# Performance work log

Measured on AMD Instinct MI355X. Metric: run time of the kernel, lower is better.

## Reference

```python
import jax, jax.numpy as jnp
import numpy as np

B, N, C, H, W = 32, 32, 3, 32, 32
HID, OUT = 256, 128


def _conv(x, w, b):
    y = jax.lax.conv_general_dilated(
        x, w, window_strides=(1, 1), padding="SAME",
        dimension_numbers=("NCHW", "OIHW", "NCHW"))
    return y + b[None, :, None, None]


def _sage(h, lw, lb, rw):
    # PyG SAGEConv with mean aggregation on a fully-connected graph (no self-loops):
    # agg_i = (sum_j h_j - h_i) / (N-1); out = agg @ lw.T + lb + h @ rw.T
    n = h.shape[1]
    agg = (jnp.sum(h, axis=1, keepdims=True) - h) / (n - 1)
    return jnp.einsum('bnd,od->bno', agg, lw) + lb + jnp.einsum('bnd,od->bno', h, rw)


def setup_inputs() -> dict:
    key = jax.random.key(0)
    ks = jax.random.split(key, 16)
    def g(k, shape, scale):
        return jax.random.normal(k, shape, dtype=jnp.float32) * scale
    return {
        "x": jax.random.normal(ks[0], (B, N, C, H, W), dtype=jnp.float32),
        "mask": jnp.ones((B, N), dtype=jnp.float32),
        "conv1_w": g(ks[1], (64, C, 3, 3), 0.1),
        "conv1_b": jnp.zeros((64,), jnp.float32),
        "conv2_w": g(ks[2], (128, 64, 3, 3), 0.05),
        "conv2_b": jnp.zeros((128,), jnp.float32),
        "fc_w": g(ks[3], (HID, 128), 0.08),
        "fc_b": jnp.zeros((HID,), jnp.float32),
        "s1_lw": g(ks[4], (HID, HID), 0.06),
        "s1_lb": jnp.zeros((HID,), jnp.float32),
        "s1_rw": g(ks[5], (HID, HID), 0.06),
        "s2_lw": g(ks[6], (OUT, HID), 0.06),
        "s2_lb": jnp.zeros((OUT,), jnp.float32),
        "s2_rw": g(ks[7], (OUT, HID), 0.06),
    }


def reference(x, mask, conv1_w, conv1_b, conv2_w, conv2_b, fc_w, fc_b,
              s1_lw, s1_lb, s1_rw, s2_lw, s2_lb, s2_rw):
    b, n, c, h, w = x.shape
    z = x.reshape(b * n, c, h, w)
    z = jax.nn.relu(_conv(z, conv1_w, conv1_b))
    z = jax.nn.relu(_conv(z, conv2_w, conv2_b))
    z = jnp.mean(z, axis=(2, 3))                      # AdaptiveAvgPool2d((1,1)) + flatten
    z = z @ fc_w.T + fc_b                             # [B*N, HID]
    z = z.reshape(b, n, -1) * mask[:, :, None]
    z = jax.nn.relu(_sage(z, s1_lw, s1_lb, s1_rw))
    z = _sage(z, s2_lw, s2_lb, s2_rw)                 # [B, N, OUT]
    return z
```

## Files before the change

kernel.cpp:

```cpp
#include <hip/hip_runtime.h>
#include <hip/hip_bf16.h>


typedef __attribute__((ext_vector_type(8))) short bfrag;
typedef __attribute__((ext_vector_type(4))) float f32x4;
typedef __attribute__((ext_vector_type(16))) float f32x16;

static __device__ __forceinline__ unsigned short f2bf(float f) {
    union { float f; unsigned u; } v; v.f = f;
    unsigned r = v.u + 0x7fff + ((v.u >> 16) & 1);
    return (unsigned short)(r >> 16);
}

static __device__ __forceinline__ unsigned cvtpk(float lo, float hi) {
    unsigned r;
    asm("v_cvt_pk_bf16_f32 %0, %1, %2" : "=v"(r) : "v"(lo), "v"(hi));
    return r;
}

static __device__ __forceinline__ void gl_lds16(const short* g, short* l) {
    __builtin_amdgcn_global_load_lds(
        (const __attribute__((address_space(1))) unsigned int*)g,
        (__attribute__((address_space(3))) unsigned int*)l, 16, 0, 0);
}

__global__ __launch_bounds__(256) void prep_kernel(
    const float* __restrict__ s1lw, const float* __restrict__ s1rw,
    const float* __restrict__ s2lw, const float* __restrict__ s2rw,
    const float* __restrict__ c2w, const float* __restrict__ c1w,
    const float* __restrict__ c1b, const float* __restrict__ fcw,
    float* __restrict__ l1T, float* __restrict__ w1pT,
    float* __restrict__ l2T, float* __restrict__ w2pT,
    float* __restrict__ fwT,
    short* __restrict__ w2c, short* __restrict__ w1b) {
    int i = blockIdx.x * 256 + threadIdx.x;
    const float inv31 = 1.f / 31.f;
    if (i < 65536) {
        int d = i >> 8, o = i & 255;
        float lw = s1lw[o * 256 + d];
        l1T[i]  = lw;
        w1pT[i] = s1rw[o * 256 + d] - lw * inv31;
    }
    if (i < 32768) {
        int d = i >> 7, o = i & 127;
        float lw = s2lw[o * 256 + d];
        l2T[i]  = lw;
        w2pT[i] = s2rw[o * 256 + d] - lw * inv31;
        int c = i >> 8, o2 = i & 255;
        fwT[i] = fcw[o2 * 128 + c];
    }
    if (i < 73728) {
        int tap = i >> 13, r = i & 8191;
        int ks = r >> 11, hi = (r >> 10) & 1, oc = (r >> 3) & 127, j = i & 7;
        int ic = ks * 16 + hi * 8 + j;
        w2c[i] = (short)f2bf(c2w[(oc * 64 + ic) * 9 + tap]);
    }
    if (i < 2048) {
        int oc = i >> 5, k = i & 31;
        float v = (k < 27) ? c1w[oc * 27 + k] : (k == 27 ? c1b[oc] : 0.f);
        w1b[i] = (short)f2bf(v);
    }
}

__global__ __launch_bounds__(256, 2) void fused_conv_kernel(
    const float* __restrict__ x, const short* __restrict__ w1b,
    const short* __restrict__ w2c, const float* __restrict__ b2,
    float* __restrict__ pooled4) {
    const int band = blockIdx.x, img = blockIdx.y;
    __shared__ short xt[3 * 12 * 34];
    __shared__ short c1t[10 * 34 * 72];
    __shared__ short bufB[3][4096];
    __shared__ float wsum[4][128];
    const int t = threadIdx.x;
    const int w = t >> 6, lane = t & 63;
    const int ln15 = lane & 15, q8 = (lane >> 4) * 8;
    const int ln31 = lane & 31, hi = lane >> 5;

    const float* xi = x + img * 3072;
    for (int idx = t; idx < 1224; idx += 256) {
        int c = idx / 408, rem = idx % 408, r = rem / 34, col = rem % 34;
        int y = band * 8 - 2 + r, xx = col - 1;
        float v = 0.f;
        if ((unsigned)y < 32u && (unsigned)xx < 32u) v = xi[c * 1024 + y * 32 + xx];
        xt[idx] = (short)f2bf(v);
    }
    {
        f32x4 z = {0.f, 0.f, 0.f, 0.f};
        for (int i = t; i < 180; i += 256) {
            int r = i / 18, rem = i % 18, side = rem / 9, q = rem % 9;
            *(f32x4*)(c1t + (r * 34 + side * 33) * 72 + q * 8) = z;
        }
    }
    bfrag b1f[4];
#pragma unroll
    for (int ot = 0; ot < 4; ++ot)
        b1f[ot] = *(const bfrag*)(w1b + (ot * 16 + ln15) * 32 + q8);

    int xOff[8]; int kMask[8]; int kOvr[8];
#pragma unroll
    for (int j = 0; j < 8; ++j) {
        int k = q8 + j;
        int c = (k * 57) >> 9;
        int rem = k - 9 * c;
        int dy = (rem * 11) >> 5;
        int dx = rem - 3 * dy;
        int cc = c < 3 ? c : 2;
        xOff[j] = cc * 408 + dy * 34 + dx;
        kMask[j] = (c < 3) ? 0xFFFF : 0;
        kOvr[j]  = (c < 3) ? 0 : (k == 27 ? 0x3F80 : 0);
    }
    __syncthreads();

    {
        const short* src = w2c + t * 8;
        short* dst = (short*)bufB + t * 8;
        gl_lds16(src, dst);
        gl_lds16(src + 2048, dst + 2048);
        gl_lds16(src + 4096, dst + 4096);
        gl_lds16(src + 6144, dst + 6144);
    }

#pragma unroll 1
    for (int pt = 0; pt < 5; ++pt) {
        const int tile = w * 5 + pt;
        const int r = tile >> 1, xcb = (tile & 1) << 4;
        const int baseA = r * 34 + xcb + ln15;
        bfrag a1f;
#pragma unroll
        for (int j = 0; j < 8; ++j)
            a1f[j] = (short)((xt[xOff[j] + baseA] & kMask[j]) | kOvr[j]);
        f32x4 acc1[4];
#pragma unroll
        for (int ot = 0; ot < 4; ++ot) {
#pragma unroll
            for (int rg = 0; rg < 4; ++rg) acc1[ot][rg] = 0.f;
            acc1[ot] = __builtin_amdgcn_mfma_f32_16x16x32_bf16(
                b1f[ot], a1f, acc1[ot], 0, 0, 0);
        }
        const int y = band * 8 - 1 + r;
        const bool valid = (unsigned)y < 32u;
        const int waddr = (r * 34 + xcb + ln15 + 1) * 72 + (lane >> 4) * 4;
#pragma unroll
        for (int ot = 0; ot < 4; ++ot) {
            uint2 pk = {0u, 0u};
            if (valid) {
                pk.x = cvtpk(fmaxf(acc1[ot][0], 0.f), fmaxf(acc1[ot][1], 0.f));
                pk.y = cvtpk(fmaxf(acc1[ot][2], 0.f), fmaxf(acc1[ot][3], 0.f));
            }
            *(uint2*)&c1t[waddr + ot * 16] = pk;
        }
    }
    __syncthreads();

    float b2v[4];
#pragma unroll
    for (int ot = 0; ot < 4; ++ot) b2v[ot] = b2[ot * 32 + ln31];

    f32x16 acc[2][4];
#pragma unroll
    for (int pt = 0; pt < 2; ++pt)
#pragma unroll
        for (int ot = 0; ot < 4; ++ot)
#pragma unroll
            for (int rg = 0; rg < 16; ++rg) acc[pt][ot][rg] = 0.f;

    const int aB0 = (w * 2 * 34 + ln31) * 72 + hi * 8;
    const int aB1 = aB0 + 34 * 72;
    const int bOff = hi * 1024 + ln31 * 8;
    const short* stSrc = w2c + t * 8;
    short* stDst = (short*)bufB + t * 8;

    auto stage = [&](int st) {
        const short* src = stSrc + st * 4096;
        short* dst = stDst + (st % 3) * 4096;
        gl_lds16(src, dst);
        gl_lds16(src + 2048, dst + 2048);
    };
    auto prefB = [&](bfrag* bf, int st) {
        const short* bc = (const short*)bufB + (st % 3) * 4096 + bOff;
#pragma unroll
        for (int kk = 0; kk < 2; ++kk)
#pragma unroll
            for (int ot = 0; ot < 4; ++ot)
                bf[kk * 4 + ot] = *(const bfrag*)(bc + kk * 2048 + ot * 256);
    };
    auto body = [&](int st, const bfrag* bCur, bfrag* bNext) {
        if (st + 2 < 18) stage(st + 2);
        const int tap = st >> 1, kh = st & 1;
        const int dy = (tap * 11) >> 5, dx = tap - 3 * dy;
        const int aOff = (dy * 34 + dx) * 72 + kh * 32;
        bfrag af0 = *(const bfrag*)&c1t[aB0 + aOff];
        bfrag af1 = *(const bfrag*)&c1t[aB0 + aOff + 16];
        bfrag af2 = *(const bfrag*)&c1t[aB1 + aOff];
        bfrag af3 = *(const bfrag*)&c1t[aB1 + aOff + 16];
        if (st + 1 < 18) prefB(bNext, st + 1);
        __builtin_amdgcn_s_setprio(1);
#pragma unroll
        for (int ot = 0; ot < 4; ++ot)
            acc[0][ot] = __builtin_amdgcn_mfma_f32_32x32x16_bf16(
                af0, bCur[ot], acc[0][ot], 0, 0, 0);
#pragma unroll
        for (int ot = 0; ot < 4; ++ot)
            acc[0][ot] = __builtin_amdgcn_mfma_f32_32x32x16_bf16(
                af1, bCur[4 + ot], acc[0][ot], 0, 0, 0);
#pragma unroll
        for (int ot = 0; ot < 4; ++ot)
            acc[1][ot] = __builtin_amdgcn_mfma_f32_32x32x16_bf16(
                af2, bCur[ot], acc[1][ot], 0, 0, 0);
#pragma unroll
        for (int ot = 0; ot < 4; ++ot)
            acc[1][ot] = __builtin_amdgcn_mfma_f32_32x32x16_bf16(
                af3, bCur[4 + ot], acc[1][ot], 0, 0, 0);
        __builtin_amdgcn_s_setprio(0);
        asm volatile("s_waitcnt vmcnt(0)" ::: "memory");
        __builtin_amdgcn_s_barrier();
    };

    bfrag bX[8], bY[8];
    prefB(bX, 0);
#pragma unroll 1
    for (int st = 0; st < 18; st += 2) {
        body(st, bX, bY);
        body(st + 1, bY, bX);
    }

#pragma unroll
    for (int ot = 0; ot < 4; ++ot) {
        float s = 0.f;
#pragma unroll
        for (int pt = 0; pt < 2; ++pt)
#pragma unroll
            for (int rg = 0; rg < 16; ++rg)
                s += fmaxf(acc[pt][ot][rg] + b2v[ot], 0.f);
        s += __shfl_xor(s, 32, 64);
        if (lane < 32) wsum[w][ot * 32 + ln31] = s;
    }
    __syncthreads();
    if (t < 128) {
        pooled4[((size_t)img * 4 + band) * 128 + t] =
            wsum[0][t] + wsum[1][t] + wsum[2][t] + wsum[3][t];
    }
}

__global__ __launch_bounds__(256) void fc_kernel(
    const float* __restrict__ pooled4, const float* __restrict__ fwT,
    const float* __restrict__ fb, const float* __restrict__ mask,
    float* __restrict__ z1) {
    const int img = blockIdx.x;
    __shared__ float m[128];
    const int t = threadIdx.x;
    if (t < 128) {
        const float* p = pooled4 + (size_t)img * 4 * 128 + t;
        m[t] = (p[0] + p[128] + p[256] + p[384]) * (1.f / 1024.f);
    }
    __syncthreads();
    float acc = fb[t];
#pragma unroll 4
    for (int c = 0; c < 128; ++c) acc = fmaf(m[c], fwT[c * 256 + t], acc);
    z1[img * 256 + t] = acc * mask[img];
}

__global__ __launch_bounds__(256) void sage1_kernel(
    const float* __restrict__ z1, const float* __restrict__ l1T,
    const float* __restrict__ lb, const float* __restrict__ w1pT,
    float* __restrict__ z2) {
    const int bb = blockIdx.x >> 3, chunk = blockIdx.x & 7;
    __shared__ float h[32 * 256];
    __shared__ float sl[256];
    const int t = threadIdx.x;
    const float* zb = z1 + bb * 8192;
    for (int idx = t; idx < 8192; idx += 256) h[idx] = zb[idx];
    __syncthreads();
    float s = 0.f;
#pragma unroll
    for (int n = 0; n < 32; ++n) s += h[n * 256 + t];
    sl[t] = s * (1.f / 31.f);
    __syncthreads();
    float c = lb[t];
#pragma unroll 4
    for (int d = 0; d < 256; ++d) c = fmaf(sl[d], l1T[d * 256 + t], c);
    float acc[4];
#pragma unroll
    for (int i = 0; i < 4; ++i) acc[i] = c;
    for (int d0 = 0; d0 < 256; d0 += 4) {
        float wv0 = w1pT[(d0 + 0) * 256 + t];
        float wv1 = w1pT[(d0 + 1) * 256 + t];
        float wv2 = w1pT[(d0 + 2) * 256 + t];
        float wv3 = w1pT[(d0 + 3) * 256 + t];
#pragma unroll
        for (int i = 0; i < 4; ++i) {
            f32x4 hv = *(const f32x4*)&h[(chunk * 4 + i) * 256 + d0];
            acc[i] = fmaf(hv[0], wv0, acc[i]);
            acc[i] = fmaf(hv[1], wv1, acc[i]);
            acc[i] = fmaf(hv[2], wv2, acc[i]);
            acc[i] = fmaf(hv[3], wv3, acc[i]);
        }
    }
    for (int i = 0; i < 4; ++i)
        z2[(bb * 32 + chunk * 4 + i) * 256 + t] = fmaxf(acc[i], 0.f);
}

__global__ __launch_bounds__(256) void sage2_kernel(
    const float* __restrict__ z2, const float* __restrict__ l2T,
    const float* __restrict__ lb, const float* __restrict__ w2pT,
    float* __restrict__ out) {
    const int bb = blockIdx.x >> 3, chunk = blockIdx.x & 7;
    __shared__ float h[32 * 256];
    __shared__ float sl[256];
    const int t = threadIdx.x;
    const float* zb = z2 + bb * 8192;
    for (int idx = t; idx < 8192; idx += 256) h[idx] = zb[idx];
    __syncthreads();
    float s = 0.f;
#pragma unroll
    for (int n = 0; n < 32; ++n) s += h[n * 256 + t];
    sl[t] = s * (1.f / 31.f);
    __syncthreads();
    const int o = t & 127, half = t >> 7;
    float c = lb[o];
#pragma unroll 4
    for (int d = 0; d < 256; ++d) c = fmaf(sl[d], l2T[d * 128 + o], c);
    float acc[2];
    acc[0] = c; acc[1] = c;
    const int n0 = chunk * 4 + half * 2;
    for (int d0 = 0; d0 < 256; d0 += 4) {
        float wv0 = w2pT[(d0 + 0) * 128 + o];
        float wv1 = w2pT[(d0 + 1) * 128 + o];
        float wv2 = w2pT[(d0 + 2) * 128 + o];
        float wv3 = w2pT[(d0 + 3) * 128 + o];
#pragma unroll
        for (int ii = 0; ii < 2; ++ii) {
            f32x4 hv = *(const f32x4*)&h[(n0 + ii) * 256 + d0];
            acc[ii] = fmaf(hv[0], wv0, acc[ii]);
            acc[ii] = fmaf(hv[1], wv1, acc[ii]);
            acc[ii] = fmaf(hv[2], wv2, acc[ii]);
            acc[ii] = fmaf(hv[3], wv3, acc[ii]);
        }
    }
    for (int ii = 0; ii < 2; ++ii)
        out[(size_t)(bb * 32 + n0 + ii) * 128 + o] = acc[ii];
}

extern "C" void kernel_launch(void* const* d_in, const int* in_sizes, int n_in,
                              void* d_out, int out_size, void* d_ws, size_t ws_size,
                              hipStream_t stream) {
    const float* x    = (const float*)d_in[0];
    const float* mask = (const float*)d_in[1];
    const float* c1w  = (const float*)d_in[2];
    const float* c1b  = (const float*)d_in[3];
    const float* c2w  = (const float*)d_in[4];
    const float* c2b  = (const float*)d_in[5];
    const float* fcw  = (const float*)d_in[6];
    const float* fcb  = (const float*)d_in[7];
    const float* s1lw = (const float*)d_in[8];
    const float* s1lb = (const float*)d_in[9];
    const float* s1rw = (const float*)d_in[10];
    const float* s2lw = (const float*)d_in[11];
    const float* s2lb = (const float*)d_in[12];
    const float* s2rw = (const float*)d_in[13];
    float* out = (float*)d_out;

    char* ws = (char*)d_ws;
    float* pooled4 = (float*)(ws);
    float* z1      = (float*)(ws + 2048u * 1024);
    float* z2      = (float*)(ws + 3072u * 1024);
    float* l1T     = (float*)(ws + 4096u * 1024);
    float* w1pT    = (float*)(ws + 4352u * 1024);
    float* l2T     = (float*)(ws + 4608u * 1024);
    float* w2pT    = (float*)(ws + 4736u * 1024);
    float* fwT     = (float*)(ws + 4864u * 1024);
    short* w2c     = (short*)(ws + 4992u * 1024);
    short* w1b     = (short*)(ws + 5136u * 1024);

    prep_kernel<<<dim3(288), 256, 0, stream>>>(s1lw, s1rw, s2lw, s2rw, c2w, c1w, c1b,
                                               fcw, l1T, w1pT, l2T, w2pT, fwT, w2c, w1b);
    fused_conv_kernel<<<dim3(4, 1024), 256, 0, stream>>>(x, w1b, w2c, c2b, pooled4);
    fc_kernel<<<dim3(1024), 256, 0, stream>>>(pooled4, fwT, fcb, mask, z1);
    sage1_kernel<<<dim3(256), 256, 0, stream>>>(z1, l1T, s1lb, w1pT, z2);
    sage2_kernel<<<dim3(256), 256, 0, stream>>>(z2, l2T, s2lb, w2pT, out);
}
```

Baseline: 280.0 us.

## Split conv2 weight staging: half via LDS, half loaded directly to registers

```diff
diff --git a/kernel.cpp b/kernel.cpp
--- a/kernel.cpp
+++ b/kernel.cpp
@@ -69,7 +69,7 @@
     const int band = blockIdx.x, img = blockIdx.y;
     __shared__ short xt[3 * 12 * 34];
     __shared__ short c1t[10 * 34 * 72];
-    __shared__ short bufB[3][4096];
+    __shared__ short bufB[3][2048];
     __shared__ float wsum[4][128];
     const int t = threadIdx.x;
     const int w = t >> 6, lane = t & 63;
@@ -111,14 +111,11 @@
     }
     __syncthreads();
 
-    {
-        const short* src = w2c + t * 8;
-        short* dst = (short*)bufB + t * 8;
-        gl_lds16(src, dst);
-        gl_lds16(src + 2048, dst + 2048);
-        gl_lds16(src + 4096, dst + 4096);
-        gl_lds16(src + 6144, dst + 6144);
-    }
+    const short* stSrc = w2c + t * 8;
+    short* stDst = (short*)bufB + t * 8;
+
+    gl_lds16(stSrc, stDst);
+    gl_lds16(stSrc + 4096, stDst + 2048);
 
 #pragma unroll 1
     for (int pt = 0; pt < 5; ++pt) {
@@ -167,25 +164,18 @@
     const int aB0 = (w * 2 * 34 + ln31) * 72 + hi * 8;
     const int aB1 = aB0 + 34 * 72;
     const int bOff = hi * 1024 + ln31 * 8;
-    const short* stSrc = w2c + t * 8;
-    short* stDst = (short*)bufB + t * 8;
 
     auto stage = [&](int st) {
-        const short* src = stSrc + st * 4096;
-        short* dst = stDst + (st % 3) * 4096;
-        gl_lds16(src, dst);
-        gl_lds16(src + 2048, dst + 2048);
+        gl_lds16(stSrc + st * 4096, stDst + (st % 3) * 2048);
     };
-    auto prefB = [&](bfrag* bf, int st) {
-        const short* bc = (const short*)bufB + (st % 3) * 4096 + bOff;
-#pragma unroll
-        for (int kk = 0; kk < 2; ++kk)
-#pragma unroll
-            for (int ot = 0; ot < 4; ++ot)
-                bf[kk * 4 + ot] = *(const bfrag*)(bc + kk * 2048 + ot * 256);
+    auto loadBG = [&](bfrag* bg, int st) {
+        const short* p = w2c + st * 4096 + 2048 + bOff;
+#pragma unroll
+        for (int ot = 0; ot < 4; ++ot) bg[ot] = *(const bfrag*)(p + ot * 256);
     };
-    auto body = [&](int st, const bfrag* bCur, bfrag* bNext) {
+    auto body = [&](int st, const bfrag* bgc, bfrag* bgn) {
         if (st + 2 < 18) stage(st + 2);
+        if (st + 1 < 18) loadBG(bgn, st + 1);
         const int tap = st >> 1, kh = st & 1;
         const int dy = (tap * 11) >> 5, dx = tap - 3 * dy;
         const int aOff = (dy * 34 + dx) * 72 + kh * 32;
@@ -193,35 +183,40 @@
         bfrag af1 = *(const bfrag*)&c1t[aB0 + aOff + 16];
         bfrag af2 = *(const bfrag*)&c1t[aB1 + aOff];
         bfrag af3 = *(const bfrag*)&c1t[aB1 + aOff + 16];
-        if (st + 1 < 18) prefB(bNext, st + 1);
+        const short* bl = (const short*)bufB + (st % 3) * 2048 + bOff;
+        bfrag bl0 = *(const bfrag*)(bl);
+        bfrag bl1 = *(const bfrag*)(bl + 256);
+        bfrag bl2 = *(const bfrag*)(bl + 512);
+        bfrag bl3 = *(const bfrag*)(bl + 768);
         __builtin_amdgcn_s_setprio(1);
-#pragma unroll
-        for (int ot = 0; ot < 4; ++ot)
-            acc[0][ot] = __builtin_amdgcn_mfma_f32_32x32x16_bf16(
-                af0, bCur[ot], acc[0][ot], 0, 0, 0);
-#pragma unroll
-        for (int ot = 0; ot < 4; ++ot)
-            acc[0][ot] = __builtin_amdgcn_mfma_f32_32x32x16_bf16(
-                af1, bCur[4 + ot], acc[0][ot], 0, 0, 0);
-#pragma unroll
-        for (int ot = 0; ot < 4; ++ot)
-            acc[1][ot] = __builtin_amdgcn_mfma_f32_32x32x16_bf16(
-                af2, bCur[ot], acc[1][ot], 0, 0, 0);
-#pragma unroll
-        for (int ot = 0; ot < 4; ++ot)
-            acc[1][ot] = __builtin_amdgcn_mfma_f32_32x32x16_bf16(
-                af3, bCur[4 + ot], acc[1][ot], 0, 0, 0);
+        acc[0][0] = __builtin_amdgcn_mfma_f32_32x32x16_bf16(af1, bgc[0], acc[0][0], 0, 0, 0);
+        acc[0][1] = __builtin_amdgcn_mfma_f32_32x32x16_bf16(af1, bgc[1], acc[0][1], 0, 0, 0);
+        acc[0][2] = __builtin_amdgcn_mfma_f32_32x32x16_bf16(af1, bgc[2], acc[0][2], 0, 0, 0);
+        acc[0][3] = __builtin_amdgcn_mfma_f32_32x32x16_bf16(af1, bgc[3], acc[0][3], 0, 0, 0);
+        acc[1][0] = __builtin_amdgcn_mfma_f32_32x32x16_bf16(af3, bgc[0], acc[1][0], 0, 0, 0);
+        acc[1][1] = __builtin_amdgcn_mfma_f32_32x32x16_bf16(af3, bgc[1], acc[1][1], 0, 0, 0);
+        acc[1][2] = __builtin_amdgcn_mfma_f32_32x32x16_bf16(af3, bgc[2], acc[1][2], 0, 0, 0);
+        acc[1][3] = __builtin_amdgcn_mfma_f32_32x32x16_bf16(af3, bgc[3], acc[1][3], 0, 0, 0);
+        acc[0][0] = __builtin_amdgcn_mfma_f32_32x32x16_bf16(af0, bl0, acc[0][0], 0, 0, 0);
+        acc[0][1] = __builtin_amdgcn_mfma_f32_32x32x16_bf16(af0, bl1, acc[0][1], 0, 0, 0);
+        acc[0][2] = __builtin_amdgcn_mfma_f32_32x32x16_bf16(af0, bl2, acc[0][2], 0, 0, 0);
+        acc[0][3] = __builtin_amdgcn_mfma_f32_32x32x16_bf16(af0, bl3, acc[0][3], 0, 0, 0);
+        acc[1][0] = __builtin_amdgcn_mfma_f32_32x32x16_bf16(af2, bl0, acc[1][0], 0, 0, 0);
+        acc[1][1] = __builtin_amdgcn_mfma_f32_32x32x16_bf16(af2, bl1, acc[1][1], 0, 0, 0);
+        acc[1][2] = __builtin_amdgcn_mfma_f32_32x32x16_bf16(af2, bl2, acc[1][2], 0, 0, 0);
+        acc[1][3] = __builtin_amdgcn_mfma_f32_32x32x16_bf16(af2, bl3, acc[1][3], 0, 0, 0);
         __builtin_amdgcn_s_setprio(0);
-        asm volatile("s_waitcnt vmcnt(0)" ::: "memory");
+        if (st < 16) { asm volatile("s_waitcnt vmcnt(4)" ::: "memory"); }
+        else         { asm volatile("s_waitcnt vmcnt(0)" ::: "memory"); }
         __builtin_amdgcn_s_barrier();
     };
 
-    bfrag bX[8], bY[8];
-    prefB(bX, 0);
+    bfrag bGX[4], bGY[4];
+    loadBG(bGX, 0);
 #pragma unroll 1
     for (int st = 0; st < 18; st += 2) {
-        body(st, bX, bY);
-        body(st + 1, bY, bX);
+        body(st, bGX, bGY);
+        body(st + 1, bGY, bGX);
     }
 
 #pragma unroll
```

Measured after the change: 293.8 us. 1.05x slower.
